# Kernel tuning notes

Hardware: AMD Instinct MI355X
Metric: run time of the kernel (lower is better)

## Reference

```python
import jax, jax.numpy as jnp
import numpy as np

N_NODES = 100000
N_EDGES = 1200000
IN_DIM = 128
HID = 64
BATCH = 8192


def setup_inputs() -> dict:
    key = jax.random.key(0)
    ks = jax.random.split(key, 8)
    x = jax.random.normal(ks[0], (N_NODES, IN_DIM), dtype=jnp.float32)
    edge_index = jax.random.randint(ks[1], (2, N_EDGES), 0, N_NODES, dtype=jnp.int64)
    user_nodes = jax.random.randint(ks[2], (BATCH,), 0, N_NODES, dtype=jnp.int64)
    movie_nodes = jax.random.randint(ks[3], (BATCH,), 0, N_NODES, dtype=jnp.int64)
    # Glorot-like init for weights, zeros for biases (as in GCNConv / nn.Linear defaults)
    W1 = jax.random.normal(ks[4], (HID, IN_DIM), dtype=jnp.float32) * (1.0 / np.sqrt(IN_DIM))
    b1 = jnp.zeros((HID,), dtype=jnp.float32)
    W2 = jax.random.normal(ks[5], (HID, HID), dtype=jnp.float32) * (1.0 / np.sqrt(HID))
    b2 = jnp.zeros((HID,), dtype=jnp.float32)
    fc_w = jax.random.normal(ks[6], (1, HID), dtype=jnp.float32) * (1.0 / np.sqrt(HID))
    fc_b = jnp.zeros((1,), dtype=jnp.float32)
    return {"x": x, "edge_index": edge_index, "user_nodes": user_nodes,
            "movie_nodes": movie_nodes, "W1": W1, "b1": b1, "W2": W2, "b2": b2,
            "fc_w": fc_w, "fc_b": fc_b}


def _gcn_conv(x, src, dst, norm, W, b, n_nodes):
    # GCNConv: linear transform first, then normalized sum-aggregation, then bias.
    h = x @ W.T                                   # [N, out]
    msg = h[src] * norm[:, None]                  # gather + scale  [E+N, out]
    out = jax.ops.segment_sum(msg, dst, num_segments=n_nodes)  # scatter-add
    return out + b


def reference(x, edge_index, user_nodes, movie_nodes, W1, b1, W2, b2, fc_w, fc_b):
    n = x.shape[0]
    # add self-loops (GCNConv default add_self_loops=True)
    loop = jnp.arange(n, dtype=edge_index.dtype)
    src = jnp.concatenate([edge_index[0], loop])
    dst = jnp.concatenate([edge_index[1], loop])
    # symmetric normalization: deg computed on destination (in-degree incl. self-loop)
    deg = jax.ops.segment_sum(jnp.ones_like(src, dtype=x.dtype), dst, num_segments=n)
    dinv = jnp.where(deg > 0, jax.lax.rsqrt(deg), 0.0)
    norm = dinv[src] * dinv[dst]                  # [E+N]
    # stacked conv -> relu (dropout is identity in eval)
    h = jax.nn.relu(_gcn_conv(x, src, dst, norm, W1, b1, n))
    h = jax.nn.relu(_gcn_conv(h, src, dst, norm, W2, b2, n))
    # predict_pairs: gather, elementwise product, linear, squeeze
    interaction = h[user_nodes] * h[movie_nodes]  # [B, HID]
    scores = (interaction @ fc_w.T + fc_b)[:, 0]  # [B]
    return scores
```

## Files before the change

### kernel.cpp

```cpp
#include <hip/hip_runtime.h>

#define HID 64

#define QS1   4096.0f
#define QINV1 (1.0f/4096.0f)
#define QH1   2048.0f
#define QS2   2048.0f
#define QINV2 (1.0f/2048.0f)

__global__ void __launch_bounds__(256) hist_kernel(
    const int4* __restrict__ dst4, int* __restrict__ hist, int n4, int nblk, int nb, int epb4) {
    __shared__ int h[512];
    const int tid = threadIdx.x, blk = blockIdx.x;
    h[tid] = 0; h[tid + 256] = 0;
    __syncthreads();
    const int beg4 = blk * epb4;
    const int end4 = min(n4, beg4 + epb4);
    for (int j = beg4 + tid; j < end4; j += 256) {
        int4 d = dst4[j];
        atomicAdd(&h[d.x >> 8], 1);
        atomicAdd(&h[d.y >> 8], 1);
        atomicAdd(&h[d.z >> 8], 1);
        atomicAdd(&h[d.w >> 8], 1);
    }
    __syncthreads();
    for (int b = tid; b < nb; b += 256) hist[b * nblk + blk] = h[b];
}

__global__ void __launch_bounds__(1024) scan_partial_kernel(
    const int* __restrict__ in, int* __restrict__ tmp, int* __restrict__ bsum, int n) {
    __shared__ int sm[1024];
    const int tid = threadIdx.x;
    int i0 = blockIdx.x * 2048 + tid * 2;
    int a = (i0 < n) ? in[i0] : 0;
    int b = (i0 + 1 < n) ? in[i0 + 1] : 0;
    int v = a + b;
    sm[tid] = v;
    __syncthreads();
#pragma unroll
    for (int off = 1; off < 1024; off <<= 1) {
        int t = (tid >= off) ? sm[tid - off] : 0;
        __syncthreads();
        sm[tid] += t;
        __syncthreads();
    }
    int excl = sm[tid] - v;
    if (i0 < n) tmp[i0] = excl;
    if (i0 + 1 < n) tmp[i0 + 1] = excl + a;
    if (tid == 1023) bsum[blockIdx.x] = sm[1023];
}

__global__ void __launch_bounds__(128) scan_sums_kernel(
    const int* __restrict__ bsum, int* __restrict__ boff, int nb) {
    __shared__ int sm[128];
    const int tid = threadIdx.x;
    int v = (tid < nb) ? bsum[tid] : 0;
    sm[tid] = v;
    __syncthreads();
#pragma unroll
    for (int off = 1; off < 128; off <<= 1) {
        int t = (tid >= off) ? sm[tid - off] : 0;
        __syncthreads();
        sm[tid] += t;
        __syncthreads();
    }
    boff[tid] = sm[tid] - v;
}

__device__ __forceinline__ int scanned_at(const int* tmp, const int* boff, int idx) {
    return tmp[idx] + boff[idx >> 11];
}

__global__ void __launch_bounds__(256) partition_kernel(
    const int4* __restrict__ src4, const int4* __restrict__ dst4,
    const int* __restrict__ tmp, const int* __restrict__ boff,
    int* __restrict__ sorted, int n4, int nblk, int nb, int epb4) {
    __shared__ int cur[512];
    const int tid = threadIdx.x, blk = blockIdx.x;
    for (int b = tid; b < nb; b += 256) cur[b] = scanned_at(tmp, boff, b * nblk + blk);
    __syncthreads();
    const int beg4 = blk * epb4;
    const int end4 = min(n4, beg4 + epb4);
    for (int j = beg4 + tid; j < end4; j += 256) {
        int4 d = dst4[j];
        int4 s = src4[j];
        int p0 = atomicAdd(&cur[d.x >> 8], 1);
        int p1 = atomicAdd(&cur[d.y >> 8], 1);
        int p2 = atomicAdd(&cur[d.z >> 8], 1);
        int p3 = atomicAdd(&cur[d.w >> 8], 1);
        sorted[p0] = (s.x << 8) | (d.x & 255);
        sorted[p1] = (s.y << 8) | (d.y & 255);
        sorted[p2] = (s.z << 8) | (d.z & 255);
        sorted[p3] = (s.w << 8) | (d.w & 255);
    }
}

#define BKCAP 4096
__global__ void __launch_bounds__(256) bucket_build_kernel(
    const int* __restrict__ sorted, const int* __restrict__ tmp, const int* __restrict__ boff,
    int* __restrict__ row_ptr, float* __restrict__ dinv, int* __restrict__ col,
    int nblk, int n, int n_edges) {
    __shared__ int cnt[256], sc[256], cur[256];
    __shared__ int ecache[BKCAP];
    const int b = blockIdx.x, tid = threadIdx.x;
    const int base = scanned_at(tmp, boff, b * nblk);
    const int end  = (b == gridDim.x - 1) ? n_edges : scanned_at(tmp, boff, (b + 1) * nblk);
    const int m = end - base;
    const bool fits = (m <= BKCAP);

    cnt[tid] = 0;
    __syncthreads();
    if (fits) {
        for (int e = tid; e < m; e += 256) {
            int v = sorted[base + e];
            ecache[e] = v;
            atomicAdd(&cnt[v & 255], 1);
        }
    } else {
        for (int e = base + tid; e < end; e += 256)
            atomicAdd(&cnt[sorted[e] & 255], 1);
    }
    __syncthreads();

    sc[tid] = cnt[tid];
    __syncthreads();
#pragma unroll
    for (int off = 1; off < 256; off <<= 1) {
        int t = (tid >= off) ? sc[tid - off] : 0;
        __syncthreads();
        sc[tid] += t;
        __syncthreads();
    }
    int ex = sc[tid] - cnt[tid];
    cur[tid] = ex;

    int node = b * 256 + tid;
    if (node < n) {
        row_ptr[node] = base + ex;
        dinv[node] = rsqrtf((float)(cnt[tid] + 1));
    }
    if (b == gridDim.x - 1 && tid == 0) row_ptr[n] = n_edges;
    __syncthreads();

    if (fits) {
        for (int e = tid; e < m; e += 256) {
            int v = ecache[e];
            int lp = atomicAdd(&cur[v & 255], 1);
            col[base + lp] = v >> 8;
        }
    } else {
        for (int e = base + tid; e < end; e += 256) {
            int v = sorted[e];
            int lp = atomicAdd(&cur[v & 255], 1);
            col[base + lp] = v >> 8;
        }
    }
}

template<int K>
__global__ void __launch_bounds__(256) gemm_tile_kernel(
    const float* __restrict__ X, const float* __restrict__ W,
    const float* __restrict__ dinv, short* __restrict__ outq, float qs, int n) {
    constexpr int BK = 32;
    constexpr int NKB = K / BK;
    __shared__ float As[BK][132];
    __shared__ float Bs[BK][68];

    const int t = threadIdx.x;
    const int mbase = blockIdx.x * 128;
    const int tc = t & 15;
    const int tm = t >> 4;
    const int lr = t >> 3;
    const int k4 = (t & 7) * 4;

    float acc[8][4] = {};

    for (int kb = 0; kb < NKB; ++kb) {
        __syncthreads();
#pragma unroll
        for (int h = 0; h < 4; ++h) {
            int m = lr + h * 32;
            int node = mbase + m;
            float4 v = make_float4(0.f, 0.f, 0.f, 0.f);
            if (node < n)
                v = *reinterpret_cast<const float4*>(X + (size_t)node * K + kb * BK + k4);
            As[k4 + 0][m] = v.x; As[k4 + 1][m] = v.y;
            As[k4 + 2][m] = v.z; As[k4 + 3][m] = v.w;
        }
#pragma unroll
        for (int h = 0; h < 2; ++h) {
            int c = lr + h * 32;
            float4 wv = *reinterpret_cast<const float4*>(W + (size_t)c * K + kb * BK + k4);
            Bs[k4 + 0][c] = wv.x; Bs[k4 + 1][c] = wv.y;
            Bs[k4 + 2][c] = wv.z; Bs[k4 + 3][c] = wv.w;
        }
        __syncthreads();
#pragma unroll
        for (int k = 0; k < BK; ++k) {
            float4 a0 = *reinterpret_cast<const float4*>(&As[k][tm * 8]);
            float4 a1 = *reinterpret_cast<const float4*>(&As[k][tm * 8 + 4]);
            float4 b = *reinterpret_cast<const float4*>(&Bs[k][tc * 4]);
            acc[0][0] += a0.x * b.x; acc[0][1] += a0.x * b.y; acc[0][2] += a0.x * b.z; acc[0][3] += a0.x * b.w;
            acc[1][0] += a0.y * b.x; acc[1][1] += a0.y * b.y; acc[1][2] += a0.y * b.z; acc[1][3] += a0.y * b.w;
            acc[2][0] += a0.z * b.x; acc[2][1] += a0.z * b.y; acc[2][2] += a0.z * b.z; acc[2][3] += a0.z * b.w;
            acc[3][0] += a0.w * b.x; acc[3][1] += a0.w * b.y; acc[3][2] += a0.w * b.z; acc[3][3] += a0.w * b.w;
            acc[4][0] += a1.x * b.x; acc[4][1] += a1.x * b.y; acc[4][2] += a1.x * b.z; acc[4][3] += a1.x * b.w;
            acc[5][0] += a1.y * b.x; acc[5][1] += a1.y * b.y; acc[5][2] += a1.y * b.z; acc[5][3] += a1.y * b.w;
            acc[6][0] += a1.z * b.x; acc[6][1] += a1.z * b.y; acc[6][2] += a1.z * b.z; acc[6][3] += a1.z * b.w;
            acc[7][0] += a1.w * b.x; acc[7][1] += a1.w * b.y; acc[7][2] += a1.w * b.z; acc[7][3] += a1.w * b.w;
        }
    }

#pragma unroll
    for (int i = 0; i < 8; ++i) {
        int node = mbase + tm * 8 + i;
        if (node < n) {
            float s = dinv[node] * qs;
            int q0 = __float2int_rn(fminf(fmaxf(acc[i][0] * s, -32767.f), 32767.f));
            int q1 = __float2int_rn(fminf(fmaxf(acc[i][1] * s, -32767.f), 32767.f));
            int q2 = __float2int_rn(fminf(fmaxf(acc[i][2] * s, -32767.f), 32767.f));
            int q3 = __float2int_rn(fminf(fmaxf(acc[i][3] * s, -32767.f), 32767.f));
            int2 pk;
            pk.x = (q0 & 0xffff) | (q1 << 16);
            pk.y = (q2 & 0xffff) | (q3 << 16);
            *reinterpret_cast<int2*>(outq + (size_t)node * HID + tc * 4) = pk;
        }
    }
}

__global__ void __launch_bounds__(256) gemm_tile_q_kernel(
    const short* __restrict__ Xq, const float* __restrict__ W,
    const float* __restrict__ dinv, short* __restrict__ outq, float qs, int n) {
    constexpr int K = 64, BK = 32, NKB = 2;
    __shared__ float As[BK][132];
    __shared__ float Bs[BK][68];

    const int t = threadIdx.x;
    const int mbase = blockIdx.x * 128;
    const int tc = t & 15;
    const int tm = t >> 4;
    const int lr = t >> 3;
    const int k4 = (t & 7) * 4;

    float acc[8][4] = {};

    for (int kb = 0; kb < NKB; ++kb) {
        __syncthreads();
#pragma unroll
        for (int h = 0; h < 4; ++h) {
            int m = lr + h * 32;
            int node = mbase + m;
            int2 raw = make_int2(0, 0);
            if (node < n)
                raw = *reinterpret_cast<const int2*>(Xq + (size_t)node * K + kb * BK + k4);
            As[k4 + 0][m] = (float)((raw.x << 16) >> 16);
            As[k4 + 1][m] = (float)(raw.x >> 16);
            As[k4 + 2][m] = (float)((raw.y << 16) >> 16);
            As[k4 + 3][m] = (float)(raw.y >> 16);
        }
#pragma unroll
        for (int h = 0; h < 2; ++h) {
            int c = lr + h * 32;
            float4 wv = *reinterpret_cast<const float4*>(W + (size_t)c * K + kb * BK + k4);
            Bs[k4 + 0][c] = wv.x; Bs[k4 + 1][c] = wv.y;
            Bs[k4 + 2][c] = wv.z; Bs[k4 + 3][c] = wv.w;
        }
        __syncthreads();
#pragma unroll
        for (int k = 0; k < BK; ++k) {
            float4 a0 = *reinterpret_cast<const float4*>(&As[k][tm * 8]);
            float4 a1 = *reinterpret_cast<const float4*>(&As[k][tm * 8 + 4]);
            float4 b = *reinterpret_cast<const float4*>(&Bs[k][tc * 4]);
            acc[0][0] += a0.x * b.x; acc[0][1] += a0.x * b.y; acc[0][2] += a0.x * b.z; acc[0][3] += a0.x * b.w;
            acc[1][0] += a0.y * b.x; acc[1][1] += a0.y * b.y; acc[1][2] += a0.y * b.z; acc[1][3] += a0.y * b.w;
            acc[2][0] += a0.z * b.x; acc[2][1] += a0.z * b.y; acc[2][2] += a0.z * b.z; acc[2][3] += a0.z * b.w;
            acc[3][0] += a0.w * b.x; acc[3][1] += a0.w * b.y; acc[3][2] += a0.w * b.z; acc[3][3] += a0.w * b.w;
            acc[4][0] += a1.x * b.x; acc[4][1] += a1.x * b.y; acc[4][2] += a1.x * b.z; acc[4][3] += a1.x * b.w;
            acc[5][0] += a1.y * b.x; acc[5][1] += a1.y * b.y; acc[5][2] += a1.y * b.z; acc[5][3] += a1.y * b.w;
            acc[6][0] += a1.z * b.x; acc[6][1] += a1.z * b.y; acc[6][2] += a1.z * b.z; acc[6][3] += a1.z * b.w;
            acc[7][0] += a1.w * b.x; acc[7][1] += a1.w * b.y; acc[7][2] += a1.w * b.z; acc[7][3] += a1.w * b.w;
        }
    }

#pragma unroll
    for (int i = 0; i < 8; ++i) {
        int node = mbase + tm * 8 + i;
        if (node < n) {
            float s = dinv[node] * qs;
            int q0 = __float2int_rn(fminf(fmaxf(acc[i][0] * s, -32767.f), 32767.f));
            int q1 = __float2int_rn(fminf(fmaxf(acc[i][1] * s, -32767.f), 32767.f));
            int q2 = __float2int_rn(fminf(fmaxf(acc[i][2] * s, -32767.f), 32767.f));
            int q3 = __float2int_rn(fminf(fmaxf(acc[i][3] * s, -32767.f), 32767.f));
            int2 pk;
            pk.x = (q0 & 0xffff) | (q1 << 16);
            pk.y = (q2 & 0xffff) | (q3 << 16);
            *reinterpret_cast<int2*>(outq + (size_t)node * HID + tc * 4) = pk;
        }
    }
}

__device__ __forceinline__ float4 gather_node_q(
    const int2* __restrict__ hq, const int* __restrict__ row_ptr, const int* __restrict__ col,
    const float* __restrict__ dinv, float4 bv, float qinv, int node, int cl) {
    int beg = row_ptr[node];
    int end = row_ptr[node + 1];

    int2 sp = hq[(size_t)node * 16 + cl];
    int4 a0 = make_int4((sp.x << 16) >> 16, sp.x >> 16, (sp.y << 16) >> 16, sp.y >> 16);
    int4 a1 = make_int4(0, 0, 0, 0);
    int4 a2 = make_int4(0, 0, 0, 0);
    int4 a3 = make_int4(0, 0, 0, 0);

    int e = beg;
    for (; e + 8 <= end; e += 8) {
        int s0 = col[e], s1 = col[e + 1], s2 = col[e + 2], s3 = col[e + 3];
        int s4 = col[e + 4], s5 = col[e + 5], s6 = col[e + 6], s7 = col[e + 7];
        int2 v0 = hq[(size_t)s0 * 16 + cl];
        int2 v1 = hq[(size_t)s1 * 16 + cl];
        int2 v2 = hq[(size_t)s2 * 16 + cl];
        int2 v3 = hq[(size_t)s3 * 16 + cl];
        int2 v4 = hq[(size_t)s4 * 16 + cl];
        int2 v5 = hq[(size_t)s5 * 16 + cl];
        int2 v6 = hq[(size_t)s6 * 16 + cl];
        int2 v7 = hq[(size_t)s7 * 16 + cl];
        a0.x += (v0.x << 16) >> 16; a0.y += v0.x >> 16; a0.z += (v0.y << 16) >> 16; a0.w += v0.y >> 16;
        a1.x += (v1.x << 16) >> 16; a1.y += v1.x >> 16; a1.z += (v1.y << 16) >> 16; a1.w += v1.y >> 16;
        a2.x += (v2.x << 16) >> 16; a2.y += v2.x >> 16; a2.z += (v2.y << 16) >> 16; a2.w += v2.y >> 16;
        a3.x += (v3.x << 16) >> 16; a3.y += v3.x >> 16; a3.z += (v3.y << 16) >> 16; a3.w += v3.y >> 16;
        a0.x += (v4.x << 16) >> 16; a0.y += v4.x >> 16; a0.z += (v4.y << 16) >> 16; a0.w += v4.y >> 16;
        a1.x += (v5.x << 16) >> 16; a1.y += v5.x >> 16; a1.z += (v5.y << 16) >> 16; a1.w += v5.y >> 16;
        a2.x += (v6.x << 16) >> 16; a2.y += v6.x >> 16; a2.z += (v6.y << 16) >> 16; a2.w += v6.y >> 16;
        a3.x += (v7.x << 16) >> 16; a3.y += v7.x >> 16; a3.z += (v7.y << 16) >> 16; a3.w += v7.y >> 16;
    }
    for (; e + 4 <= end; e += 4) {
        int s0 = col[e], s1 = col[e + 1], s2 = col[e + 2], s3 = col[e + 3];
        int2 v0 = hq[(size_t)s0 * 16 + cl];
        int2 v1 = hq[(size_t)s1 * 16 + cl];
        int2 v2 = hq[(size_t)s2 * 16 + cl];
        int2 v3 = hq[(size_t)s3 * 16 + cl];
        a0.x += (v0.x << 16) >> 16; a0.y += v0.x >> 16; a0.z += (v0.y << 16) >> 16; a0.w += v0.y >> 16;
        a1.x += (v1.x << 16) >> 16; a1.y += v1.x >> 16; a1.z += (v1.y << 16) >> 16; a1.w += v1.y >> 16;
        a2.x += (v2.x << 16) >> 16; a2.y += v2.x >> 16; a2.z += (v2.y << 16) >> 16; a2.w += v2.y >> 16;
        a3.x += (v3.x << 16) >> 16; a3.y += v3.x >> 16; a3.z += (v3.y << 16) >> 16; a3.w += v3.y >> 16;
    }
    for (; e < end; ++e) {
        int2 v = hq[(size_t)col[e] * 16 + cl];
        a0.x += (v.x << 16) >> 16; a0.y += v.x >> 16; a0.z += (v.y << 16) >> 16; a0.w += v.y >> 16;
    }

    float sq = dinv[node] * qinv;
    float4 r;
    r.x = fmaf((float)((a0.x + a1.x) + (a2.x + a3.x)), sq, bv.x);
    r.y = fmaf((float)((a0.y + a1.y) + (a2.y + a3.y)), sq, bv.y);
    r.z = fmaf((float)((a0.z + a1.z) + (a2.z + a3.z)), sq, bv.z);
    r.w = fmaf((float)((a0.w + a1.w) + (a2.w + a3.w)), sq, bv.w);
    r.x = r.x > 0.f ? r.x : 0.f;
    r.y = r.y > 0.f ? r.y : 0.f;
    r.z = r.z > 0.f ? r.z : 0.f;
    r.w = r.w > 0.f ? r.w : 0.f;
    return r;
}

__global__ void __launch_bounds__(256) gather_kernel(
    const short* __restrict__ hsq, const int* __restrict__ row_ptr, const int* __restrict__ col,
    const float* __restrict__ dinv, const float* __restrict__ b, float qinv, float qh,
    short* __restrict__ outq, int n) {
    const int2* __restrict__ hq = (const int2*)hsq;
    const int lane = threadIdx.x & 63;
    const int sub = lane >> 4;
    const int cl  = lane & 15;
    const int wv = blockIdx.x * 4 + (threadIdx.x >> 6);
    const int nwv = gridDim.x * 4;
    const int ngroups = (n + 3) >> 2;

    float4 bv = ((const float4*)b)[cl];

    for (int g = wv; g < ngroups; g += nwv) {
        int node = g * 4 + sub;
        if (node >= n) continue;
        float4 r = gather_node_q(hq, row_ptr, col, dinv, bv, qinv, node, cl);
        int q0 = __float2int_rn(fminf(r.x * qh, 32767.f));
        int q1 = __float2int_rn(fminf(r.y * qh, 32767.f));
        int q2 = __float2int_rn(fminf(r.z * qh, 32767.f));
        int q3 = __float2int_rn(fminf(r.w * qh, 32767.f));
        int2 pk;
        pk.x = (q0 & 0xffff) | (q1 << 16);
        pk.y = (q2 & 0xffff) | (q3 << 16);
        *((int2*)outq + (size_t)node * 16 + cl) = pk;
    }
}

__global__ void __launch_bounds__(256) gather_final_kernel(
    const short* __restrict__ hsq, const int* __restrict__ row_ptr, const int* __restrict__ col,
    const int* __restrict__ users, const int* __restrict__ movies,
    const float* __restrict__ dinv, const float* __restrict__ b, float qinv,
    const float* __restrict__ fc_w, const float* __restrict__ fc_b,
    float* __restrict__ out, int batch) {
    const int2* __restrict__ hq = (const int2*)hsq;
    const int lane = threadIdx.x & 63;
    const int sub = lane >> 4;
    const int cl  = lane & 15;
    const int g = blockIdx.x * 4 + (threadIdx.x >> 6);

    int pair = g * 2 + (sub >> 1);
    int node = 0;
    if (pair < batch) node = ((sub & 1) == 0) ? users[pair] : movies[pair];

    float4 bv = ((const float4*)b)[cl];
    float4 r = gather_node_q(hq, row_ptr, col, dinv, bv, qinv, node, cl);

    float4 fw = ((const float4*)fc_w)[cl];
    float px = __shfl_xor(r.x, 16, 64);
    float py = __shfl_xor(r.y, 16, 64);
    float pz = __shfl_xor(r.z, 16, 64);
    float pw = __shfl_xor(r.w, 16, 64);
    float s = r.x * px * fw.x + r.y * py * fw.y + r.z * pz * fw.z + r.w * pw * fw.w;
#pragma unroll
    for (int off = 1; off < 16; off <<= 1)
        s += __shfl_xor(s, off, 64);

    if ((lane & 31) == 0) {
        int pr = g * 2 + (lane >> 5);
        if (pr < batch) out[pr] = s + fc_b[0];
    }
}

extern "C" void kernel_launch(void* const* d_in, const int* in_sizes, int n_in,
                              void* d_out, int out_size, void* d_ws, size_t ws_size,
                              hipStream_t stream) {
    const float* x     = (const float*)d_in[0];
    const int*   edge  = (const int*)d_in[1];
    const int*   users = (const int*)d_in[2];
    const int*   movies= (const int*)d_in[3];
    const float* W1    = (const float*)d_in[4];
    const float* b1    = (const float*)d_in[5];
    const float* W2    = (const float*)d_in[6];
    const float* b2    = (const float*)d_in[7];
    const float* fc_w  = (const float*)d_in[8];
    const float* fc_b  = (const float*)d_in[9];
    float* out = (float*)d_out;

    const int IN_DIM = 128;
    const int n       = in_sizes[0] / IN_DIM;
    const int n_edges = in_sizes[1] / 2;
    const int batch   = in_sizes[2];

    const int* esrc = edge;
    const int* edst = edge + n_edges;

    const int n4   = n_edges / 4;
    const int NBLK = 512;
    const int EPB4 = (n4 + NBLK - 1) / NBLK;
    const int NB   = (n + 255) >> 8;
    const int HLEN = NB * NBLK;
    const int SB   = (HLEN + 2047) / 2048;

    char* ws = (char*)d_ws;
    size_t o = 0;
    auto alloc = [&](size_t bytes) { void* p = ws + o; o = (o + bytes + 255) & ~(size_t)255; return p; };
    int*   hist    = (int*)  alloc(sizeof(int) * HLEN);
    int*   tmp     = (int*)  alloc(sizeof(int) * HLEN);
    int*   bsum    = (int*)  alloc(sizeof(int) * 128);
    int*   boff    = (int*)  alloc(sizeof(int) * 128);
    int*   sorted  = (int*)  alloc(sizeof(int) * n_edges);
    int*   col     = (int*)  alloc(sizeof(int) * n_edges);
    int*   row_ptr = (int*)  alloc(sizeof(int) * (n + 1));
    float* dinv    = (float*)alloc(sizeof(float) * n);
    short* Bq      = (short*)alloc(sizeof(short) * (size_t)n * HID);
    short* Hq      = (short*)alloc(sizeof(short) * (size_t)n * HID);

    hist_kernel<<<NBLK, 256, 0, stream>>>((const int4*)edst, hist, n4, NBLK, NB, EPB4);
    scan_partial_kernel<<<SB, 1024, 0, stream>>>(hist, tmp, bsum, HLEN);
    scan_sums_kernel<<<1, 128, 0, stream>>>(bsum, boff, SB);
    partition_kernel<<<NBLK, 256, 0, stream>>>((const int4*)esrc, (const int4*)edst,
                                               tmp, boff, sorted, n4, NBLK, NB, EPB4);
    bucket_build_kernel<<<NB, 256, 0, stream>>>(sorted, tmp, boff, row_ptr, dinv, col,
                                                NBLK, n, n_edges);

    const int gather_blocks = 3125;
    const int head_blocks = (batch + 7) / 8;

    gemm_tile_kernel<128><<<(n + 127) / 128, 256, 0, stream>>>(x, W1, dinv, Bq, QS1, n);
    gather_kernel<<<gather_blocks, 256, 0, stream>>>(Bq, row_ptr, col, dinv, b1,
                                                     QINV1, QH1, Hq, n);

    gemm_tile_q_kernel<<<(n + 127) / 128, 256, 0, stream>>>(Hq, W2, dinv, Bq, QS2 / QH1, n);
    gather_final_kernel<<<head_blocks, 256, 0, stream>>>(Bq, row_ptr, col, users, movies,
                                                         dinv, b2, QINV2, fc_w, fc_b,
                                                         out, batch);

}
```

Before: 145.4 us.

## Fuse CSR build into one cooperative kernel with grid syncs; unloop gather grid

```diff
diff --git a/kernel.cpp b/kernel.cpp
--- a/kernel.cpp
+++ b/kernel.cpp
@@ -1,4 +1,7 @@
 #include <hip/hip_runtime.h>
+#include <hip/hip_cooperative_groups.h>
+
+namespace cg = cooperative_groups;
 
 #define HID 64
 
@@ -8,151 +11,145 @@
 #define QS2   2048.0f
 #define QINV2 (1.0f/2048.0f)
 
-__global__ void __launch_bounds__(256) hist_kernel(
-    const int4* __restrict__ dst4, int* __restrict__ hist, int n4, int nblk, int nb, int epb4) {
-    __shared__ int h[512];
+#define NBLKC 512
+#define BKCAP 4096
+
+__global__ void __launch_bounds__(256) build_fused_kernel(
+    const int4* __restrict__ src4, const int4* __restrict__ dst4,
+    int* __restrict__ hist, int* __restrict__ tmp, int* __restrict__ bsum, int* __restrict__ boff,
+    int* __restrict__ sorted, int* __restrict__ row_ptr, float* __restrict__ dinv,
+    int* __restrict__ col, int n4, int n, int n_edges, int epb4, int nb) {
+    cg::grid_group grid = cg::this_grid();
+    __shared__ int S[768 + BKCAP];
     const int tid = threadIdx.x, blk = blockIdx.x;
-    h[tid] = 0; h[tid + 256] = 0;
-    __syncthreads();
     const int beg4 = blk * epb4;
     const int end4 = min(n4, beg4 + epb4);
+
+    S[tid] = 0; S[tid + 256] = 0;
+    __syncthreads();
     for (int j = beg4 + tid; j < end4; j += 256) {
         int4 d = dst4[j];
-        atomicAdd(&h[d.x >> 8], 1);
-        atomicAdd(&h[d.y >> 8], 1);
-        atomicAdd(&h[d.z >> 8], 1);
-        atomicAdd(&h[d.w >> 8], 1);
+        atomicAdd(&S[d.x >> 8], 1);
+        atomicAdd(&S[d.y >> 8], 1);
+        atomicAdd(&S[d.z >> 8], 1);
+        atomicAdd(&S[d.w >> 8], 1);
     }
     __syncthreads();
-    for (int b = tid; b < nb; b += 256) hist[b * nblk + blk] = h[b];
-}
-
-__global__ void __launch_bounds__(1024) scan_partial_kernel(
-    const int* __restrict__ in, int* __restrict__ tmp, int* __restrict__ bsum, int n) {
-    __shared__ int sm[1024];
-    const int tid = threadIdx.x;
-    int i0 = blockIdx.x * 2048 + tid * 2;
-    int a = (i0 < n) ? in[i0] : 0;
-    int b = (i0 + 1 < n) ? in[i0 + 1] : 0;
-    int v = a + b;
-    sm[tid] = v;
+    for (int b = tid; b < nb; b += 256) hist[b * NBLKC + blk] = S[b];
+    grid.sync();
+
+    if (blk < nb) {
+        int i0 = blk * NBLKC + tid * 2;
+        int a = hist[i0], bb = hist[i0 + 1];
+        int v = a + bb;
+        S[tid] = v;
+        __syncthreads();
+#pragma unroll
+        for (int off = 1; off < 256; off <<= 1) {
+            int t = (tid >= off) ? S[tid - off] : 0;
+            __syncthreads();
+            S[tid] += t;
+            __syncthreads();
+        }
+        int excl = S[tid] - v;
+        tmp[i0] = excl;
+        tmp[i0 + 1] = excl + a;
+        if (tid == 255) bsum[blk] = S[255];
+    }
+    grid.sync();
+
+    if (blk == 0) {
+        int i0 = tid * 2;
+        int a = (i0 < nb) ? bsum[i0] : 0;
+        int bb = (i0 + 1 < nb) ? bsum[i0 + 1] : 0;
+        int v = a + bb;
+        S[tid] = v;
+        __syncthreads();
+#pragma unroll
+        for (int off = 1; off < 256; off <<= 1) {
+            int t = (tid >= off) ? S[tid - off] : 0;
+            __syncthreads();
+            S[tid] += t;
+            __syncthreads();
+        }
+        int excl = S[tid] - v;
+        if (i0 < nb) boff[i0] = excl;
+        if (i0 + 1 < nb) boff[i0 + 1] = excl + a;
+    }
+    grid.sync();
+
+    for (int b = tid; b < nb; b += 256) S[b] = tmp[b * NBLKC + blk] + boff[b];
     __syncthreads();
-#pragma unroll
-    for (int off = 1; off < 1024; off <<= 1) {
-        int t = (tid >= off) ? sm[tid - off] : 0;
-        __syncthreads();
-        sm[tid] += t;
-        __syncthreads();
-    }
-    int excl = sm[tid] - v;
-    if (i0 < n) tmp[i0] = excl;
-    if (i0 + 1 < n) tmp[i0 + 1] = excl + a;
-    if (tid == 1023) bsum[blockIdx.x] = sm[1023];
-}
-
-__global__ void __launch_bounds__(128) scan_sums_kernel(
-    const int* __restrict__ bsum, int* __restrict__ boff, int nb) {
-    __shared__ int sm[128];
-    const int tid = threadIdx.x;
-    int v = (tid < nb) ? bsum[tid] : 0;
-    sm[tid] = v;
-    __syncthreads();
-#pragma unroll
-    for (int off = 1; off < 128; off <<= 1) {
-        int t = (tid >= off) ? sm[tid - off] : 0;
-        __syncthreads();
-        sm[tid] += t;
-        __syncthreads();
-    }
-    boff[tid] = sm[tid] - v;
-}
-
-__device__ __forceinline__ int scanned_at(const int* tmp, const int* boff, int idx) {
-    return tmp[idx] + boff[idx >> 11];
-}
-
-__global__ void __launch_bounds__(256) partition_kernel(
-    const int4* __restrict__ src4, const int4* __restrict__ dst4,
-    const int* __restrict__ tmp, const int* __restrict__ boff,
-    int* __restrict__ sorted, int n4, int nblk, int nb, int epb4) {
-    __shared__ int cur[512];
-    const int tid = threadIdx.x, blk = blockIdx.x;
-    for (int b = tid; b < nb; b += 256) cur[b] = scanned_at(tmp, boff, b * nblk + blk);
-    __syncthreads();
-    const int beg4 = blk * epb4;
-    const int end4 = min(n4, beg4 + epb4);
     for (int j = beg4 + tid; j < end4; j += 256) {
         int4 d = dst4[j];
         int4 s = src4[j];
-        int p0 = atomicAdd(&cur[d.x >> 8], 1);
-        int p1 = atomicAdd(&cur[d.y >> 8], 1);
-        int p2 = atomicAdd(&cur[d.z >> 8], 1);
-        int p3 = atomicAdd(&cur[d.w >> 8], 1);
+        int p0 = atomicAdd(&S[d.x >> 8], 1);
+        int p1 = atomicAdd(&S[d.y >> 8], 1);
+        int p2 = atomicAdd(&S[d.z >> 8], 1);
+        int p3 = atomicAdd(&S[d.w >> 8], 1);
         sorted[p0] = (s.x << 8) | (d.x & 255);
         sorted[p1] = (s.y << 8) | (d.y & 255);
         sorted[p2] = (s.z << 8) | (d.z & 255);
         sorted[p3] = (s.w << 8) | (d.w & 255);
     }
-}
-
-#define BKCAP 4096
-__global__ void __launch_bounds__(256) bucket_build_kernel(
-    const int* __restrict__ sorted, const int* __restrict__ tmp, const int* __restrict__ boff,
-    int* __restrict__ row_ptr, float* __restrict__ dinv, int* __restrict__ col,
-    int nblk, int n, int n_edges) {
-    __shared__ int cnt[256], sc[256], cur[256];
-    __shared__ int ecache[BKCAP];
-    const int b = blockIdx.x, tid = threadIdx.x;
-    const int base = scanned_at(tmp, boff, b * nblk);
-    const int end  = (b == gridDim.x - 1) ? n_edges : scanned_at(tmp, boff, (b + 1) * nblk);
-    const int m = end - base;
-    const bool fits = (m <= BKCAP);
-
-    cnt[tid] = 0;
-    __syncthreads();
-    if (fits) {
-        for (int e = tid; e < m; e += 256) {
-            int v = sorted[base + e];
-            ecache[e] = v;
-            atomicAdd(&cnt[v & 255], 1);
-        }
-    } else {
-        for (int e = base + tid; e < end; e += 256)
-            atomicAdd(&cnt[sorted[e] & 255], 1);
-    }
-    __syncthreads();
-
-    sc[tid] = cnt[tid];
-    __syncthreads();
-#pragma unroll
-    for (int off = 1; off < 256; off <<= 1) {
-        int t = (tid >= off) ? sc[tid - off] : 0;
-        __syncthreads();
-        sc[tid] += t;
-        __syncthreads();
-    }
-    int ex = sc[tid] - cnt[tid];
-    cur[tid] = ex;
-
-    int node = b * 256 + tid;
-    if (node < n) {
-        row_ptr[node] = base + ex;
-        dinv[node] = rsqrtf((float)(cnt[tid] + 1));
-    }
-    if (b == gridDim.x - 1 && tid == 0) row_ptr[n] = n_edges;
-    __syncthreads();
-
-    if (fits) {
-        for (int e = tid; e < m; e += 256) {
-            int v = ecache[e];
-            int lp = atomicAdd(&cur[v & 255], 1);
-            col[base + lp] = v >> 8;
-        }
-    } else {
-        for (int e = base + tid; e < end; e += 256) {
-            int v = sorted[e];
-            int lp = atomicAdd(&cur[v & 255], 1);
-            col[base + lp] = v >> 8;
+    grid.sync();
+
+    if (blk < nb) {
+        int* cnt = S;
+        int* sc = S + 256;
+        int* cur = S + 512;
+        int* ecache = S + 768;
+        const int base = tmp[blk * NBLKC] + boff[blk];
+        const int end = (blk == nb - 1) ? n_edges : (tmp[(blk + 1) * NBLKC] + boff[blk + 1]);
+        const int m = end - base;
+        const bool fits = (m <= BKCAP);
+
+        cnt[tid] = 0;
+        __syncthreads();
+        if (fits) {
+            for (int e = tid; e < m; e += 256) {
+                int v = sorted[base + e];
+                ecache[e] = v;
+                atomicAdd(&cnt[v & 255], 1);
+            }
+        } else {
+            for (int e = base + tid; e < end; e += 256)
+                atomicAdd(&cnt[sorted[e] & 255], 1);
+        }
+        __syncthreads();
+
+        sc[tid] = cnt[tid];
+        __syncthreads();
+#pragma unroll
+        for (int off = 1; off < 256; off <<= 1) {
+            int t = (tid >= off) ? sc[tid - off] : 0;
+            __syncthreads();
+            sc[tid] += t;
+            __syncthreads();
+        }
+        int ex = sc[tid] - cnt[tid];
+        cur[tid] = ex;
+
+        int node = blk * 256 + tid;
+        if (node < n) {
+            row_ptr[node] = base + ex;
+            dinv[node] = rsqrtf((float)(cnt[tid] + 1));
+        }
+        if (blk == nb - 1 && tid == 0) row_ptr[n] = n_edges;
+        __syncthreads();
+
+        if (fits) {
+            for (int e = tid; e < m; e += 256) {
+                int v = ecache[e];
+                int lp = atomicAdd(&cur[v & 255], 1);
+                col[base + lp] = v >> 8;
+            }
+        } else {
+            for (int e = base + tid; e < end; e += 256) {
+                int v = sorted[e];
+                int lp = atomicAdd(&cur[v & 255], 1);
+                col[base + lp] = v >> 8;
+            }
         }
     }
 }
@@ -369,25 +366,20 @@
     const int lane = threadIdx.x & 63;
     const int sub = lane >> 4;
     const int cl  = lane & 15;
-    const int wv = blockIdx.x * 4 + (threadIdx.x >> 6);
-    const int nwv = gridDim.x * 4;
-    const int ngroups = (n + 3) >> 2;
-
+    const int g = blockIdx.x * 4 + (threadIdx.x >> 6);
+
+    int node = g * 4 + sub;
+    if (node >= n) return;
     float4 bv = ((const float4*)b)[cl];
-
-    for (int g = wv; g < ngroups; g += nwv) {
-        int node = g * 4 + sub;
-        if (node >= n) continue;
-        float4 r = gather_node_q(hq, row_ptr, col, dinv, bv, qinv, node, cl);
-        int q0 = __float2int_rn(fminf(r.x * qh, 32767.f));
-        int q1 = __float2int_rn(fminf(r.y * qh, 32767.f));
-        int q2 = __float2int_rn(fminf(r.z * qh, 32767.f));
-        int q3 = __float2int_rn(fminf(r.w * qh, 32767.f));
-        int2 pk;
-        pk.x = (q0 & 0xffff) | (q1 << 16);
-        pk.y = (q2 & 0xffff) | (q3 << 16);
-        *((int2*)outq + (size_t)node * 16 + cl) = pk;
-    }
+    float4 r = gather_node_q(hq, row_ptr, col, dinv, bv, qinv, node, cl);
+    int q0 = __float2int_rn(fminf(r.x * qh, 32767.f));
+    int q1 = __float2int_rn(fminf(r.y * qh, 32767.f));
+    int q2 = __float2int_rn(fminf(r.z * qh, 32767.f));
+    int q3 = __float2int_rn(fminf(r.w * qh, 32767.f));
+    int2 pk;
+    pk.x = (q0 & 0xffff) | (q1 << 16);
+    pk.y = (q2 & 0xffff) | (q3 << 16);
+    *((int2*)outq + (size_t)node * 16 + cl) = pk;
 }
 
 __global__ void __launch_bounds__(256) gather_final_kernel(
@@ -448,20 +440,18 @@
     const int* esrc = edge;
     const int* edst = edge + n_edges;
 
-    const int n4   = n_edges / 4;
-    const int NBLK = 512;
-    const int EPB4 = (n4 + NBLK - 1) / NBLK;
-    const int NB   = (n + 255) >> 8;
-    const int HLEN = NB * NBLK;
-    const int SB   = (HLEN + 2047) / 2048;
+    int n4   = n_edges / 4;
+    int EPB4 = (n4 + NBLKC - 1) / NBLKC;
+    int NB   = (n + 255) >> 8;
+    const int HLEN = NB * NBLKC;
 
     char* ws = (char*)d_ws;
     size_t o = 0;
     auto alloc = [&](size_t bytes) { void* p = ws + o; o = (o + bytes + 255) & ~(size_t)255; return p; };
     int*   hist    = (int*)  alloc(sizeof(int) * HLEN);
     int*   tmp     = (int*)  alloc(sizeof(int) * HLEN);
-    int*   bsum    = (int*)  alloc(sizeof(int) * 128);
-    int*   boff    = (int*)  alloc(sizeof(int) * 128);
+    int*   bsum    = (int*)  alloc(sizeof(int) * NBLKC);
+    int*   boff    = (int*)  alloc(sizeof(int) * NBLKC);
     int*   sorted  = (int*)  alloc(sizeof(int) * n_edges);
     int*   col     = (int*)  alloc(sizeof(int) * n_edges);
     int*   row_ptr = (int*)  alloc(sizeof(int) * (n + 1));
@@ -469,15 +459,20 @@
     short* Bq      = (short*)alloc(sizeof(short) * (size_t)n * HID);
     short* Hq      = (short*)alloc(sizeof(short) * (size_t)n * HID);
 
-    hist_kernel<<<NBLK, 256, 0, stream>>>((const int4*)edst, hist, n4, NBLK, NB, EPB4);
-    scan_partial_kernel<<<SB, 1024, 0, stream>>>(hist, tmp, bsum, HLEN);
-    scan_sums_kernel<<<1, 128, 0, stream>>>(bsum, boff, SB);
-    partition_kernel<<<NBLK, 256, 0, stream>>>((const int4*)esrc, (const int4*)edst,
-                                               tmp, boff, sorted, n4, NBLK, NB, EPB4);
-    bucket_build_kernel<<<NB, 256, 0, stream>>>(sorted, tmp, boff, row_ptr, dinv, col,
-                                                NBLK, n, n_edges);
-
-    const int gather_blocks = 3125;
+    {
+        const int4* src4 = (const int4*)esrc;
+        const int4* dst4 = (const int4*)edst;
+        int ne = n_edges, nn = n;
+        void* args[] = { (void*)&src4, (void*)&dst4, (void*)&hist, (void*)&tmp,
+                         (void*)&bsum, (void*)&boff, (void*)&sorted, (void*)&row_ptr,
+                         (void*)&dinv, (void*)&col, (void*)&n4, (void*)&nn,
+                         (void*)&ne, (void*)&EPB4, (void*)&NB };
+        hipLaunchCooperativeKernel((void*)build_fused_kernel, dim3(NBLKC), dim3(256),
+                                   args, 0, stream);
+    }
+
+    const int ngroups = (n + 3) >> 2;
+    const int gather_blocks = (ngroups + 3) / 4;
     const int head_blocks = (batch + 7) / 8;
 
     gemm_tile_kernel<128><<<(n + 127) / 128, 256, 0, stream>>>(x, W1, dinv, Bq, QS1, n);
@@ -488,5 +483,4 @@
     gather_final_kernel<<<head_blocks, 256, 0, stream>>>(Bq, row_ptr, col, users, movies,
                                                          dinv, b2, QINV2, fc_w, fc_b,
                                                          out, batch);
-
-}
+}
```

New measurement: 380.6 us. 2.62x slower.
